# Performance work log

Measured on AMD Instinct MI355X. Metric: run time of the kernel, lower is better.

The kernel has to match this reference:

```python
import jax, jax.numpy as jnp
import numpy as np

N = 100000   # input nodes
M = 100000   # output nodes (size = (N, M))
NNZ = 3_200_000  # edges, avg_degree 32
B = 32       # batch
D = 32       # Kaiming channel dim


def setup_inputs() -> dict:
    key = jax.random.key(0)
    k1, k2, k3 = jax.random.split(key, 3)
    # COO indices: row 0 = src (in [0, N)), row 1 = dst (in [0, M))
    indices = jax.random.randint(k1, (2, NNZ), 0, N, dtype=jnp.int32)
    # Kaiming init: randn * sqrt(2/d), as in the torch module when d is given
    values = jax.random.normal(k2, (NNZ,), dtype=jnp.float32) * np.float32((2.0 / D) ** 0.5)
    bias = jnp.zeros((M, 1), dtype=jnp.float32)
    x = jax.random.normal(k3, (B, N, 1), dtype=jnp.float32)
    return {"x": x, "indices": indices, "values": values, "bias": bias}


def reference(x, indices, values, bias):
    # Equivalent of: for each b, sparse.mm(W.T, x[b]) + bias, W in COO (N, M)
    # y[b, m] = sum_{e: dst[e]==m} values[e] * x[b, src[e]] + bias[m]
    src = indices[0]
    dst = indices[1]
    contrib = x[:, src, 0] * values[None, :]           # (B, NNZ) gather-multiply
    y = jax.ops.segment_sum(contrib.T, dst, num_segments=M)  # (M, B) scatter-add
    return (y.T + bias[:, 0][None, :])[..., None]       # (B, M, 1)
```

## Files before the change

kernel.cpp:

```cpp
#include <hip/hip_runtime.h>
#include <hip/hip_fp16.h>
#include <stdint.h>

#define NB 32
#define BIN_SHIFT 6
#define BIN_ROWS 64
#define NBINS_MAX 2048
#define FCHUNK 8192
#define FTHREADS 1024
#define EPT (FCHUNK / FTHREADS)
#define SRC_BITS 18
#define SRC_MASK ((1u << SRC_BITS) - 1)
#define CAP 2816
#define MAXK 11

__global__ void transpose_x_kernel(const float* __restrict__ x,
                                   __half* __restrict__ xt, int N) {
    __shared__ float tile[32][33];
    int n0 = blockIdx.x * 32;
    for (int i = threadIdx.y; i < 32; i += 8) {
        int n = n0 + threadIdx.x;
        tile[i][threadIdx.x] = (n < N) ? x[(size_t)i * N + n] : 0.f;
    }
    __syncthreads();
    for (int i = threadIdx.y; i < 32; i += 8) {
        int n = n0 + i;
        if (n < N) xt[(size_t)n * NB + threadIdx.x] =
            __float2half(tile[threadIdx.x][i]);
    }
}

__global__ void bin_fill(const int* __restrict__ src,
                         const int* __restrict__ dst,
                         const float* __restrict__ vals,
                         int* __restrict__ binCursor,
                         uint2* __restrict__ csr,
                         int* __restrict__ ovCount,
                         int* __restrict__ ovList,
                         int nnz, int nbins) {
    __shared__ int lhist[NBINS_MAX];
    __shared__ int lbase[NBINS_MAX];
    int t = threadIdx.x;
    int e0 = blockIdx.x * FCHUNK;
    int dcache[EPT];
    for (int i = t; i < nbins; i += FTHREADS) lhist[i] = 0;
    __syncthreads();
#pragma unroll
    for (int k = 0; k < EPT; ++k) {
        int e = e0 + k * FTHREADS + t;
        int d = (e < nnz) ? dst[e] : -1;
        dcache[k] = d;
        if (d >= 0) atomicAdd(&lhist[d >> BIN_SHIFT], 1);
    }
    __syncthreads();
    for (int i = t; i < nbins; i += FTHREADS) {
        int c = lhist[i];
        lbase[i] = c ? atomicAdd(&binCursor[i], c) : 0;
        lhist[i] = 0;
    }
    __syncthreads();
#pragma unroll
    for (int k = 0; k < EPT; ++k) {
        int e = e0 + k * FTHREADS + t;
        int d = dcache[k];
        if (d >= 0) {
            int bin = d >> BIN_SHIFT;
            int r = lbase[bin] + atomicAdd(&lhist[bin], 1);
            if (r < CAP) {
                uint32_t meta = ((uint32_t)(d & (BIN_ROWS - 1)) << SRC_BITS) |
                                (uint32_t)src[e];
                csr[(size_t)bin * CAP + r] =
                    make_uint2(meta, __float_as_uint(vals[e]));
            } else {
                int op = atomicAdd(ovCount, 1);
                ovList[op] = e;
            }
        }
    }
}

__global__ __launch_bounds__(256) void sort_gather(
        const int* __restrict__ binCursor,
        const uint2* __restrict__ csr,
        const __half* __restrict__ xt,
        const float* __restrict__ bias,
        float* __restrict__ out, int M) {
    __shared__ uint2 sorted[CAP];
    __shared__ int rowCnt[BIN_ROWS];
    __shared__ int rowOff[BIN_ROWS];
    int t = threadIdx.x;
    int bin = blockIdx.x;
    int start = bin * CAP;
    int cnt   = min(binCursor[bin], CAP);
    int g = t >> 5;
    int b = t & 31;

    uint2 reg[MAXK];
#pragma unroll
    for (int k = 0; k < MAXK; ++k) {
        int j = t + k * 256;
        if (j < cnt) reg[k] = csr[start + j];
    }
    if (t < BIN_ROWS) rowCnt[t] = 0;
    __syncthreads();
#pragma unroll
    for (int k = 0; k < MAXK; ++k) {
        int j = t + k * 256;
        if (j < cnt) atomicAdd(&rowCnt[reg[k].x >> SRC_BITS], 1);
    }
    __syncthreads();
    if (t == 0) {
        int run = 0;
#pragma unroll
        for (int r = 0; r < BIN_ROWS; ++r) {
            rowOff[r] = run;
            run += rowCnt[r];
        }
    }
    __syncthreads();
#pragma unroll
    for (int k = 0; k < MAXK; ++k) {
        int j = t + k * 256;
        if (j < cnt) {
            int p = atomicAdd(&rowOff[reg[k].x >> SRC_BITS], 1);
            sorted[p] = reg[k];
        }
    }
    __syncthreads();
    for (int r = g; r < BIN_ROWS; r += 8) {
        int m = bin * BIN_ROWS + r;
        if (m >= M) break;
        int jend = rowOff[r];
        int jj   = jend - rowCnt[r];
        float acc0 = 0.f, acc1 = 0.f;
        for (; jj + 8 <= jend; jj += 8) {
            uint2 e0 = sorted[jj + 0];
            uint2 e1 = sorted[jj + 1];
            uint2 e2 = sorted[jj + 2];
            uint2 e3 = sorted[jj + 3];
            uint2 e4 = sorted[jj + 4];
            uint2 e5 = sorted[jj + 5];
            uint2 e6 = sorted[jj + 6];
            uint2 e7 = sorted[jj + 7];
            float x0 = __half2float(xt[(size_t)(e0.x & SRC_MASK) * NB + b]);
            float x1 = __half2float(xt[(size_t)(e1.x & SRC_MASK) * NB + b]);
            float x2 = __half2float(xt[(size_t)(e2.x & SRC_MASK) * NB + b]);
            float x3 = __half2float(xt[(size_t)(e3.x & SRC_MASK) * NB + b]);
            float x4 = __half2float(xt[(size_t)(e4.x & SRC_MASK) * NB + b]);
            float x5 = __half2float(xt[(size_t)(e5.x & SRC_MASK) * NB + b]);
            float x6 = __half2float(xt[(size_t)(e6.x & SRC_MASK) * NB + b]);
            float x7 = __half2float(xt[(size_t)(e7.x & SRC_MASK) * NB + b]);
            acc0 = fmaf(__uint_as_float(e0.y), x0, acc0);
            acc1 = fmaf(__uint_as_float(e1.y), x1, acc1);
            acc0 = fmaf(__uint_as_float(e2.y), x2, acc0);
            acc1 = fmaf(__uint_as_float(e3.y), x3, acc1);
            acc0 = fmaf(__uint_as_float(e4.y), x4, acc0);
            acc1 = fmaf(__uint_as_float(e5.y), x5, acc1);
            acc0 = fmaf(__uint_as_float(e6.y), x6, acc0);
            acc1 = fmaf(__uint_as_float(e7.y), x7, acc1);
        }
        for (; jj < jend; ++jj) {
            uint2 e = sorted[jj];
            acc0 = fmaf(__uint_as_float(e.y),
                        __half2float(xt[(size_t)(e.x & SRC_MASK) * NB + b]),
                        acc0);
        }
        out[(size_t)b * M + m] = acc0 + acc1 + bias[m];
    }
}

__global__ void fixup_kernel(const int* __restrict__ ovCount,
                             const int* __restrict__ ovList,
                             const int* __restrict__ src,
                             const int* __restrict__ dst,
                             const float* __restrict__ vals,
                             const __half* __restrict__ xt,
                             float* __restrict__ out, int M) {
    long long total = (long long)(*ovCount) * 32;
    long long stride = (long long)gridDim.x * blockDim.x;
    for (long long i = (long long)blockIdx.x * blockDim.x + threadIdx.x;
         i < total; i += stride) {
        int k = (int)(i >> 5);
        int b = (int)(i & 31);
        int e = ovList[k];
        atomicAdd(&out[(size_t)b * M + dst[e]],
                  vals[e] * __half2float(xt[(size_t)src[e] * NB + b]));
    }
}

__global__ void finalize_kernel(const float* __restrict__ yt,
                                const float* __restrict__ bias,
                                float* __restrict__ out, int M) {
    __shared__ float tile[32][33];
    int m0 = blockIdx.x * 32;
    for (int i = threadIdx.y; i < 32; i += 8) {
        int m = m0 + i;
        tile[i][threadIdx.x] = (m < M) ? yt[(size_t)m * NB + threadIdx.x] : 0.f;
    }
    __syncthreads();
    for (int i = threadIdx.y; i < 32; i += 8) {
        int m = m0 + threadIdx.x;
        if (m < M) out[(size_t)i * M + m] = tile[threadIdx.x][i] + bias[m];
    }
}

__global__ void scatter_kernel(const int* __restrict__ src,
                               const int* __restrict__ dst,
                               const float* __restrict__ vals,
                               const __half* __restrict__ xt,
                               float* __restrict__ yt, int nnz) {
    long long tid = (long long)blockIdx.x * blockDim.x + threadIdx.x;
    int e = (int)(tid >> 5);
    if (e >= nnz) return;
    int b = (int)(tid & 31);
    atomicAdd(&yt[(size_t)dst[e] * NB + b],
              vals[e] * __half2float(xt[(size_t)src[e] * NB + b]));
}

extern "C" void kernel_launch(void* const* d_in, const int* in_sizes, int n_in,
                              void* d_out, int out_size, void* d_ws, size_t ws_size,
                              hipStream_t stream) {
    const float* x       = (const float*)d_in[0];
    const int*   indices = (const int*)  d_in[1];
    const float* vals    = (const float*)d_in[2];
    const float* bias    = (const float*)d_in[3];

    float* out = (float*)d_out;

    int nnz = in_sizes[1] / 2;
    int N   = in_sizes[0] / NB;
    int M   = in_sizes[3];

    const int* src = indices;
    const int* dst = indices + nnz;

    int nbins = (M + BIN_ROWS - 1) >> BIN_SHIFT;

    __half* xt       = (__half*)d_ws;
    float* yt        = (float*)(xt + (size_t)N * NB);
    int*   binCursor = (int*)(yt + (size_t)M * NB);
    int*   ovCount   = binCursor + NBINS_MAX;
    int*   ovList    = ovCount + 4;
    uint2* csr       = (uint2*)(((uintptr_t)(ovList + nnz) + 15) &
                                ~(uintptr_t)15);

    size_t need = (size_t)((char*)(csr + (size_t)nbins * CAP) - (char*)d_ws);

    transpose_x_kernel<<<(N + 31) / 32, dim3(32, 8), 0, stream>>>(x, xt, N);

    if (ws_size >= need) {
        hipMemsetAsync(binCursor, 0, (NBINS_MAX + 4) * sizeof(int), stream);
        int fgrid = (nnz + FCHUNK - 1) / FCHUNK;
        bin_fill<<<fgrid, FTHREADS, 0, stream>>>(src, dst, vals, binCursor,
                                                 csr, ovCount, ovList,
                                                 nnz, nbins);
        sort_gather<<<nbins, 256, 0, stream>>>(binCursor, csr, xt, bias,
                                               out, M);
        fixup_kernel<<<32, 256, 0, stream>>>(ovCount, ovList, src, dst, vals,
                                             xt, out, M);
    } else {
        hipMemsetAsync(yt, 0, (size_t)M * NB * sizeof(float), stream);
        long long pairs = (long long)nnz * NB;
        int grid = (int)((pairs + 255) / 256);
        scatter_kernel<<<grid, 256, 0, stream>>>(src, dst, vals, xt, yt, nnz);
        finalize_kernel<<<(M + 31) / 32, dim3(32, 8), 0, stream>>>(yt, bias,
                                                                   out, M);
    }
}
```

Measured before the change: 213.9 us.

## Replace global bin cursors with per-block segment offsets and deterministic binning

The fill kernel no longer takes global atomics on per-bin cursors. Each block computes a local exclusive scan of its bin histogram and writes its edges contiguously in its own chunk, plus a per-block offset row. The gather kernel then reads up to 391 small segments per bin and rebuilds the bin's edge list in shared memory. This removes the global atomics, the memset, and the overflow/fixup kernel. The cost is many short, scattered segment reads per bin and a per-thread serial loop over segments, and bins larger than the shared buffer fall back to a shared-memory atomic-accumulate path.

Result: slower. 263.0 us (+22.9%).

```diff
diff --git a/kernel.cpp b/kernel.cpp
--- a/kernel.cpp
+++ b/kernel.cpp
@@ -9,10 +9,10 @@
 #define FCHUNK 8192
 #define FTHREADS 1024
 #define EPT (FCHUNK / FTHREADS)
+#define FGRID_MAX 512
 #define SRC_BITS 18
 #define SRC_MASK ((1u << SRC_BITS) - 1)
 #define CAP 2816
-#define MAXK 11
 
 __global__ void transpose_x_kernel(const float* __restrict__ x,
                                    __half* __restrict__ xt, int N) {
@@ -30,161 +30,181 @@
     }
 }
 
-__global__ void bin_fill(const int* __restrict__ src,
-                         const int* __restrict__ dst,
-                         const float* __restrict__ vals,
-                         int* __restrict__ binCursor,
-                         uint2* __restrict__ csr,
-                         int* __restrict__ ovCount,
-                         int* __restrict__ ovList,
-                         int nnz, int nbins) {
+__global__ void fill_bm(const int* __restrict__ src,
+                        const int* __restrict__ dst,
+                        const float* __restrict__ vals,
+                        uint2* __restrict__ csr,
+                        int* __restrict__ segOff,
+                        int nnz, int nbins) {
     __shared__ int lhist[NBINS_MAX];
     __shared__ int lbase[NBINS_MAX];
+    __shared__ int sscan[FTHREADS];
     int t = threadIdx.x;
-    int e0 = blockIdx.x * FCHUNK;
+    int k = blockIdx.x;
+    int e0 = k * FCHUNK;
+    int chunk = min(FCHUNK, nnz - e0);
     int dcache[EPT];
-    for (int i = t; i < nbins; i += FTHREADS) lhist[i] = 0;
+
+    for (int i = t; i < NBINS_MAX; i += FTHREADS) lhist[i] = 0;
     __syncthreads();
 #pragma unroll
-    for (int k = 0; k < EPT; ++k) {
-        int e = e0 + k * FTHREADS + t;
+    for (int q = 0; q < EPT; ++q) {
+        int e = e0 + q * FTHREADS + t;
         int d = (e < nnz) ? dst[e] : -1;
-        dcache[k] = d;
+        dcache[q] = d;
         if (d >= 0) atomicAdd(&lhist[d >> BIN_SHIFT], 1);
     }
     __syncthreads();
-    for (int i = t; i < nbins; i += FTHREADS) {
-        int c = lhist[i];
-        lbase[i] = c ? atomicAdd(&binCursor[i], c) : 0;
-        lhist[i] = 0;
-    }
-    __syncthreads();
+    int s0 = lhist[2 * t];
+    int s1 = lhist[2 * t + 1];
+    int tsum = s0 + s1;
+    sscan[t] = tsum;
+    __syncthreads();
+    for (int off = 1; off < FTHREADS; off <<= 1) {
+        int add = (t >= off) ? sscan[t - off] : 0;
+        __syncthreads();
+        sscan[t] += add;
+        __syncthreads();
+    }
+    int excl = sscan[t] - tsum;
+    lbase[2 * t]     = excl;
+    lbase[2 * t + 1] = excl + s0;
+    lhist[2 * t]     = 0;
+    lhist[2 * t + 1] = 0;
+    __syncthreads();
+    int* row = segOff + (size_t)k * (nbins + 1);
+    for (int i = t; i <= nbins; i += FTHREADS)
+        row[i] = e0 + ((i < nbins) ? lbase[i] : chunk);
 #pragma unroll
-    for (int k = 0; k < EPT; ++k) {
-        int e = e0 + k * FTHREADS + t;
-        int d = dcache[k];
+    for (int q = 0; q < EPT; ++q) {
+        int e = e0 + q * FTHREADS + t;
+        int d = dcache[q];
         if (d >= 0) {
             int bin = d >> BIN_SHIFT;
             int r = lbase[bin] + atomicAdd(&lhist[bin], 1);
-            if (r < CAP) {
-                uint32_t meta = ((uint32_t)(d & (BIN_ROWS - 1)) << SRC_BITS) |
-                                (uint32_t)src[e];
-                csr[(size_t)bin * CAP + r] =
-                    make_uint2(meta, __float_as_uint(vals[e]));
-            } else {
-                int op = atomicAdd(ovCount, 1);
-                ovList[op] = e;
-            }
+            uint32_t meta = ((uint32_t)(d & (BIN_ROWS - 1)) << SRC_BITS) |
+                            (uint32_t)src[e];
+            csr[e0 + r] = make_uint2(meta, __float_as_uint(vals[e]));
         }
     }
 }
 
 __global__ __launch_bounds__(256) void sort_gather(
-        const int* __restrict__ binCursor,
+        const int* __restrict__ segOff,
         const uint2* __restrict__ csr,
         const __half* __restrict__ xt,
         const float* __restrict__ bias,
-        float* __restrict__ out, int M) {
+        float* __restrict__ out, int M, int nbins, int fgrid) {
     __shared__ uint2 sorted[CAP];
+    __shared__ int segBase[FGRID_MAX];
+    __shared__ short segCnt[FGRID_MAX];
     __shared__ int rowCnt[BIN_ROWS];
     __shared__ int rowOff[BIN_ROWS];
+    __shared__ int totS;
     int t = threadIdx.x;
     int bin = blockIdx.x;
-    int start = bin * CAP;
-    int cnt   = min(binCursor[bin], CAP);
     int g = t >> 5;
     int b = t & 31;
 
-    uint2 reg[MAXK];
+    if (t == 0) totS = 0;
+    if (t < BIN_ROWS) rowCnt[t] = 0;
+    __syncthreads();
+    int mySum = 0;
+    for (int k = t; k < fgrid; k += 256) {
+        const int* row = segOff + (size_t)k * (nbins + 1) + bin;
+        int s0 = row[0];
+        int s1 = row[1];
+        segBase[k] = s0;
+        segCnt[k] = (short)(s1 - s0);
+        mySum += s1 - s0;
+    }
+    if (mySum) atomicAdd(&totS, mySum);
+    __syncthreads();
+    int cnt = totS;
+
+    if (cnt <= CAP) {
+        for (int k = t; k < fgrid; k += 256) {
+            int base = segBase[k], n = segCnt[k];
+            for (int j = 0; j < n; ++j)
+                atomicAdd(&rowCnt[csr[base + j].x >> SRC_BITS], 1);
+        }
+        __syncthreads();
+        if (t == 0) {
+            int run = 0;
 #pragma unroll
-    for (int k = 0; k < MAXK; ++k) {
-        int j = t + k * 256;
-        if (j < cnt) reg[k] = csr[start + j];
-    }
-    if (t < BIN_ROWS) rowCnt[t] = 0;
-    __syncthreads();
-#pragma unroll
-    for (int k = 0; k < MAXK; ++k) {
-        int j = t + k * 256;
-        if (j < cnt) atomicAdd(&rowCnt[reg[k].x >> SRC_BITS], 1);
-    }
-    __syncthreads();
-    if (t == 0) {
-        int run = 0;
-#pragma unroll
-        for (int r = 0; r < BIN_ROWS; ++r) {
-            rowOff[r] = run;
-            run += rowCnt[r];
-        }
-    }
-    __syncthreads();
-#pragma unroll
-    for (int k = 0; k < MAXK; ++k) {
-        int j = t + k * 256;
-        if (j < cnt) {
-            int p = atomicAdd(&rowOff[reg[k].x >> SRC_BITS], 1);
-            sorted[p] = reg[k];
-        }
-    }
-    __syncthreads();
-    for (int r = g; r < BIN_ROWS; r += 8) {
-        int m = bin * BIN_ROWS + r;
-        if (m >= M) break;
-        int jend = rowOff[r];
-        int jj   = jend - rowCnt[r];
-        float acc0 = 0.f, acc1 = 0.f;
-        for (; jj + 8 <= jend; jj += 8) {
-            uint2 e0 = sorted[jj + 0];
-            uint2 e1 = sorted[jj + 1];
-            uint2 e2 = sorted[jj + 2];
-            uint2 e3 = sorted[jj + 3];
-            uint2 e4 = sorted[jj + 4];
-            uint2 e5 = sorted[jj + 5];
-            uint2 e6 = sorted[jj + 6];
-            uint2 e7 = sorted[jj + 7];
-            float x0 = __half2float(xt[(size_t)(e0.x & SRC_MASK) * NB + b]);
-            float x1 = __half2float(xt[(size_t)(e1.x & SRC_MASK) * NB + b]);
-            float x2 = __half2float(xt[(size_t)(e2.x & SRC_MASK) * NB + b]);
-            float x3 = __half2float(xt[(size_t)(e3.x & SRC_MASK) * NB + b]);
-            float x4 = __half2float(xt[(size_t)(e4.x & SRC_MASK) * NB + b]);
-            float x5 = __half2float(xt[(size_t)(e5.x & SRC_MASK) * NB + b]);
-            float x6 = __half2float(xt[(size_t)(e6.x & SRC_MASK) * NB + b]);
-            float x7 = __half2float(xt[(size_t)(e7.x & SRC_MASK) * NB + b]);
-            acc0 = fmaf(__uint_as_float(e0.y), x0, acc0);
-            acc1 = fmaf(__uint_as_float(e1.y), x1, acc1);
-            acc0 = fmaf(__uint_as_float(e2.y), x2, acc0);
-            acc1 = fmaf(__uint_as_float(e3.y), x3, acc1);
-            acc0 = fmaf(__uint_as_float(e4.y), x4, acc0);
-            acc1 = fmaf(__uint_as_float(e5.y), x5, acc1);
-            acc0 = fmaf(__uint_as_float(e6.y), x6, acc0);
-            acc1 = fmaf(__uint_as_float(e7.y), x7, acc1);
-        }
-        for (; jj < jend; ++jj) {
-            uint2 e = sorted[jj];
-            acc0 = fmaf(__uint_as_float(e.y),
-                        __half2float(xt[(size_t)(e.x & SRC_MASK) * NB + b]),
-                        acc0);
-        }
-        out[(size_t)b * M + m] = acc0 + acc1 + bias[m];
-    }
-}
-
-__global__ void fixup_kernel(const int* __restrict__ ovCount,
-                             const int* __restrict__ ovList,
-                             const int* __restrict__ src,
-                             const int* __restrict__ dst,
-                             const float* __restrict__ vals,
-                             const __half* __restrict__ xt,
-                             float* __restrict__ out, int M) {
-    long long total = (long long)(*ovCount) * 32;
-    long long stride = (long long)gridDim.x * blockDim.x;
-    for (long long i = (long long)blockIdx.x * blockDim.x + threadIdx.x;
-         i < total; i += stride) {
-        int k = (int)(i >> 5);
-        int b = (int)(i & 31);
-        int e = ovList[k];
-        atomicAdd(&out[(size_t)b * M + dst[e]],
-                  vals[e] * __half2float(xt[(size_t)src[e] * NB + b]));
+            for (int r = 0; r < BIN_ROWS; ++r) {
+                rowOff[r] = run;
+                run += rowCnt[r];
+            }
+        }
+        __syncthreads();
+        for (int k = t; k < fgrid; k += 256) {
+            int base = segBase[k], n = segCnt[k];
+            for (int j = 0; j < n; ++j) {
+                uint2 e = csr[base + j];
+                int p = atomicAdd(&rowOff[e.x >> SRC_BITS], 1);
+                sorted[p] = e;
+            }
+        }
+        __syncthreads();
+        for (int r = g; r < BIN_ROWS; r += 8) {
+            int m = bin * BIN_ROWS + r;
+            if (m >= M) break;
+            int jend = rowOff[r];
+            int jj   = jend - rowCnt[r];
+            float acc0 = 0.f, acc1 = 0.f;
+            for (; jj + 8 <= jend; jj += 8) {
+                uint2 e0 = sorted[jj + 0];
+                uint2 e1 = sorted[jj + 1];
+                uint2 e2 = sorted[jj + 2];
+                uint2 e3 = sorted[jj + 3];
+                uint2 e4 = sorted[jj + 4];
+                uint2 e5 = sorted[jj + 5];
+                uint2 e6 = sorted[jj + 6];
+                uint2 e7 = sorted[jj + 7];
+                float x0 = __half2float(xt[(size_t)(e0.x & SRC_MASK) * NB + b]);
+                float x1 = __half2float(xt[(size_t)(e1.x & SRC_MASK) * NB + b]);
+                float x2 = __half2float(xt[(size_t)(e2.x & SRC_MASK) * NB + b]);
+                float x3 = __half2float(xt[(size_t)(e3.x & SRC_MASK) * NB + b]);
+                float x4 = __half2float(xt[(size_t)(e4.x & SRC_MASK) * NB + b]);
+                float x5 = __half2float(xt[(size_t)(e5.x & SRC_MASK) * NB + b]);
+                float x6 = __half2float(xt[(size_t)(e6.x & SRC_MASK) * NB + b]);
+                float x7 = __half2float(xt[(size_t)(e7.x & SRC_MASK) * NB + b]);
+                acc0 = fmaf(__uint_as_float(e0.y), x0, acc0);
+                acc1 = fmaf(__uint_as_float(e1.y), x1, acc1);
+                acc0 = fmaf(__uint_as_float(e2.y), x2, acc0);
+                acc1 = fmaf(__uint_as_float(e3.y), x3, acc1);
+                acc0 = fmaf(__uint_as_float(e4.y), x4, acc0);
+                acc1 = fmaf(__uint_as_float(e5.y), x5, acc1);
+                acc0 = fmaf(__uint_as_float(e6.y), x6, acc0);
+                acc1 = fmaf(__uint_as_float(e7.y), x7, acc1);
+            }
+            for (; jj < jend; ++jj) {
+                uint2 e = sorted[jj];
+                acc0 = fmaf(__uint_as_float(e.y),
+                            __half2float(xt[(size_t)(e.x & SRC_MASK) * NB + b]),
+                            acc0);
+            }
+            out[(size_t)b * M + m] = acc0 + acc1 + bias[m];
+        }
+    } else {
+        float* tile = (float*)sorted;
+        for (int i = t; i < BIN_ROWS * NB; i += 256) tile[i] = 0.f;
+        __syncthreads();
+        for (int k = g; k < fgrid; k += 8) {
+            int base = segBase[k], n = segCnt[k];
+            for (int j = 0; j < n; ++j) {
+                uint2 e = csr[base + j];
+                float xv = __half2float(xt[(size_t)(e.x & SRC_MASK) * NB + b]);
+                atomicAdd(&tile[(e.x >> SRC_BITS) * NB + b],
+                          __uint_as_float(e.y) * xv);
+            }
+        }
+        __syncthreads();
+        for (int i = t; i < BIN_ROWS * NB; i += 256) {
+            int m = bin * BIN_ROWS + (i >> 5);
+            if (m < M) out[(size_t)(i & 31) * M + m] = tile[i] + bias[m];
+        }
     }
 }
 
@@ -235,29 +255,23 @@
     const int* dst = indices + nnz;
 
     int nbins = (M + BIN_ROWS - 1) >> BIN_SHIFT;
-
-    __half* xt       = (__half*)d_ws;
-    float* yt        = (float*)(xt + (size_t)N * NB);
-    int*   binCursor = (int*)(yt + (size_t)M * NB);
-    int*   ovCount   = binCursor + NBINS_MAX;
-    int*   ovList    = ovCount + 4;
-    uint2* csr       = (uint2*)(((uintptr_t)(ovList + nnz) + 15) &
-                                ~(uintptr_t)15);
-
-    size_t need = (size_t)((char*)(csr + (size_t)nbins * CAP) - (char*)d_ws);
+    int fgrid = (nnz + FCHUNK - 1) / FCHUNK;
+
+    __half* xt     = (__half*)d_ws;
+    float*  yt     = (float*)(xt + (size_t)N * NB);
+    int*    segOff = (int*)(yt + (size_t)M * NB);
+    uint2*  csr    = (uint2*)(((uintptr_t)(segOff +
+                        (size_t)fgrid * (nbins + 1)) + 15) & ~(uintptr_t)15);
+
+    size_t need = (size_t)((char*)(csr + nnz) - (char*)d_ws);
 
     transpose_x_kernel<<<(N + 31) / 32, dim3(32, 8), 0, stream>>>(x, xt, N);
 
-    if (ws_size >= need) {
-        hipMemsetAsync(binCursor, 0, (NBINS_MAX + 4) * sizeof(int), stream);
-        int fgrid = (nnz + FCHUNK - 1) / FCHUNK;
-        bin_fill<<<fgrid, FTHREADS, 0, stream>>>(src, dst, vals, binCursor,
-                                                 csr, ovCount, ovList,
-                                                 nnz, nbins);
-        sort_gather<<<nbins, 256, 0, stream>>>(binCursor, csr, xt, bias,
-                                               out, M);
-        fixup_kernel<<<32, 256, 0, stream>>>(ovCount, ovList, src, dst, vals,
-                                             xt, out, M);
+    if (ws_size >= need && fgrid <= FGRID_MAX && nbins <= NBINS_MAX) {
+        fill_bm<<<fgrid, FTHREADS, 0, stream>>>(src, dst, vals, csr, segOff,
+                                                nnz, nbins);
+        sort_gather<<<nbins, 256, 0, stream>>>(segOff, csr, xt, bias, out,
+                                               M, nbins, fgrid);
     } else {
         hipMemsetAsync(yt, 0, (size_t)M * NB * sizeof(float), stream);
         long long pairs = (long long)nnz * NB;
```

## Replace single-pass fine binning with two-level coarse/fine radix partition

Applied to the files above, without the earlier changes.

Edges are first scattered into 1024-row coarse buckets while per-64-row fine counts are accumulated. A scan turns those counts into exact offsets, and a second pass scatters each coarse bucket into a compact fine CSR. This is meant to reduce global atomic contention and scattered-write inefficiency from binning straight into 1563 fixed-capacity bins. It adds two kernel launches and an extra read/write pass over all edges. sort_gather gains an atomic shared-tile fallback for bins above capacity, replacing the overflow path for fine bins.

New measurement: 198.1 us. 1.08x faster.

```diff
diff --git a/kernel.cpp b/kernel.cpp
--- a/kernel.cpp
+++ b/kernel.cpp
@@ -6,13 +6,21 @@
 #define BIN_SHIFT 6
 #define BIN_ROWS 64
 #define NBINS_MAX 2048
+#define CSHIFT 10
+#define NC_MAX 128
+#define FPC 16
 #define FCHUNK 8192
 #define FTHREADS 1024
 #define EPT (FCHUNK / FTHREADS)
+#define CAP_C 34816
+#define P2CHUNK 8192
+#define CH2 ((CAP_C + P2CHUNK - 1) / P2CHUNK)
+#define EPT2 (P2CHUNK / FTHREADS)
 #define SRC_BITS 18
 #define SRC_MASK ((1u << SRC_BITS) - 1)
 #define CAP 2816
 #define MAXK 11
+
 
 __global__ void transpose_x_kernel(const float* __restrict__ x,
                                    __half* __restrict__ xt, int N) {
@@ -30,57 +38,133 @@
     }
 }
 
-__global__ void bin_fill(const int* __restrict__ src,
-                         const int* __restrict__ dst,
-                         const float* __restrict__ vals,
-                         int* __restrict__ binCursor,
-                         uint2* __restrict__ csr,
-                         int* __restrict__ ovCount,
-                         int* __restrict__ ovList,
-                         int nnz, int nbins) {
-    __shared__ int lhist[NBINS_MAX];
-    __shared__ int lbase[NBINS_MAX];
+__global__ void fill_coarse(const int* __restrict__ src,
+                            const int* __restrict__ dst,
+                            const float* __restrict__ vals,
+                            int* __restrict__ cCursor,
+                            uint2* __restrict__ cCsr,
+                            int* __restrict__ fineCnt,
+                            int* __restrict__ ovCount,
+                            int* __restrict__ ovList,
+                            int nnz, int ncoarse, int nbins) {
+    __shared__ int lhist[NC_MAX];
+    __shared__ int lbase[NC_MAX];
+    __shared__ int fh[NBINS_MAX];
     int t = threadIdx.x;
     int e0 = blockIdx.x * FCHUNK;
     int dcache[EPT];
-    for (int i = t; i < nbins; i += FTHREADS) lhist[i] = 0;
-    __syncthreads();
-#pragma unroll
-    for (int k = 0; k < EPT; ++k) {
-        int e = e0 + k * FTHREADS + t;
+    for (int i = t; i < NC_MAX; i += FTHREADS) lhist[i] = 0;
+    for (int i = t; i < nbins; i += FTHREADS) fh[i] = 0;
+    __syncthreads();
+#pragma unroll
+    for (int q = 0; q < EPT; ++q) {
+        int e = e0 + q * FTHREADS + t;
         int d = (e < nnz) ? dst[e] : -1;
-        dcache[k] = d;
-        if (d >= 0) atomicAdd(&lhist[d >> BIN_SHIFT], 1);
-    }
-    __syncthreads();
-    for (int i = t; i < nbins; i += FTHREADS) {
+        dcache[q] = d;
+        if (d >= 0) atomicAdd(&lhist[d >> CSHIFT], 1);
+    }
+    __syncthreads();
+    for (int i = t; i < ncoarse; i += FTHREADS) {
         int c = lhist[i];
-        lbase[i] = c ? atomicAdd(&binCursor[i], c) : 0;
+        lbase[i] = c ? atomicAdd(&cCursor[i], c) : 0;
         lhist[i] = 0;
     }
     __syncthreads();
 #pragma unroll
-    for (int k = 0; k < EPT; ++k) {
-        int e = e0 + k * FTHREADS + t;
-        int d = dcache[k];
+    for (int q = 0; q < EPT; ++q) {
+        int e = e0 + q * FTHREADS + t;
+        int d = dcache[q];
         if (d >= 0) {
-            int bin = d >> BIN_SHIFT;
-            int r = lbase[bin] + atomicAdd(&lhist[bin], 1);
-            if (r < CAP) {
-                uint32_t meta = ((uint32_t)(d & (BIN_ROWS - 1)) << SRC_BITS) |
+            int c = d >> CSHIFT;
+            int r = lbase[c] + atomicAdd(&lhist[c], 1);
+            if (r < CAP_C) {
+                uint32_t meta = ((uint32_t)(d & 1023) << SRC_BITS) |
                                 (uint32_t)src[e];
-                csr[(size_t)bin * CAP + r] =
+                cCsr[(size_t)c * CAP_C + r] =
                     make_uint2(meta, __float_as_uint(vals[e]));
+                atomicAdd(&fh[d >> BIN_SHIFT], 1);
             } else {
                 int op = atomicAdd(ovCount, 1);
                 ovList[op] = e;
             }
         }
     }
+    __syncthreads();
+    for (int i = t; i < nbins; i += FTHREADS)
+        if (fh[i]) atomicAdd(&fineCnt[i], fh[i]);
+}
+
+__global__ void fine_scan(const int* __restrict__ fineCnt,
+                          int* __restrict__ fineBase,
+                          int* __restrict__ fineCursor, int nbins) {
+    __shared__ int s[1024];
+    int t = threadIdx.x;
+    int i0 = t * 2, i1 = t * 2 + 1;
+    int v0 = (i0 < nbins) ? fineCnt[i0] : 0;
+    int v1 = (i1 < nbins) ? fineCnt[i1] : 0;
+    int sum = v0 + v1;
+    s[t] = sum;
+    __syncthreads();
+    for (int off = 1; off < 1024; off <<= 1) {
+        int add = (t >= off) ? s[t - off] : 0;
+        __syncthreads();
+        s[t] += add;
+        __syncthreads();
+    }
+    int run = s[t] - sum;
+    if (i0 < nbins) { fineBase[i0] = run; fineCursor[i0] = run; }
+    run += v0;
+    if (i1 < nbins) { fineBase[i1] = run; fineCursor[i1] = run; }
+}
+
+__global__ void fill_fine(const int* __restrict__ cCursor,
+                          const uint2* __restrict__ cCsr,
+                          int* __restrict__ fineCursor,
+                          uint2* __restrict__ fineCsr) {
+    __shared__ int lhist[FPC];
+    __shared__ int lbase[FPC];
+    int c = blockIdx.x / CH2;
+    int i = blockIdx.x % CH2;
+    int n  = min(cCursor[c], CAP_C);
+    int j0 = i * P2CHUNK;
+    int jn = min(j0 + P2CHUNK, n);
+    if (j0 >= jn) return;
+    int t = threadIdx.x;
+    uint2 ecache[EPT2];
+    if (t < FPC) lhist[t] = 0;
+    __syncthreads();
+    const uint2* reg = cCsr + (size_t)c * CAP_C;
+#pragma unroll
+    for (int q = 0; q < EPT2; ++q) {
+        int j = j0 + q * FTHREADS + t;
+        if (j < jn) {
+            uint2 e = reg[j];
+            ecache[q] = e;
+            atomicAdd(&lhist[(e.x >> 24) & 15], 1);
+        }
+    }
+    __syncthreads();
+    if (t < FPC) {
+        int cn = lhist[t];
+        lbase[t] = cn ? atomicAdd(&fineCursor[c * FPC + t], cn) : 0;
+        lhist[t] = 0;
+    }
+    __syncthreads();
+#pragma unroll
+    for (int q = 0; q < EPT2; ++q) {
+        int j = j0 + q * FTHREADS + t;
+        if (j < jn) {
+            uint2 e = ecache[q];
+            int f = (e.x >> 24) & 15;
+            int p = lbase[f] + atomicAdd(&lhist[f], 1);
+            fineCsr[p] = e;
+        }
+    }
 }
 
 __global__ __launch_bounds__(256) void sort_gather(
-        const int* __restrict__ binCursor,
+        const int* __restrict__ fineBase,
+        const int* __restrict__ fineCursor,
         const uint2* __restrict__ csr,
         const __half* __restrict__ xt,
         const float* __restrict__ bias,
@@ -90,82 +174,100 @@
     __shared__ int rowOff[BIN_ROWS];
     int t = threadIdx.x;
     int bin = blockIdx.x;
-    int start = bin * CAP;
-    int cnt   = min(binCursor[bin], CAP);
+    int start = fineBase[bin];
+    int cnt   = fineCursor[bin] - start;
     int g = t >> 5;
     int b = t & 31;
 
-    uint2 reg[MAXK];
-#pragma unroll
-    for (int k = 0; k < MAXK; ++k) {
-        int j = t + k * 256;
-        if (j < cnt) reg[k] = csr[start + j];
-    }
-    if (t < BIN_ROWS) rowCnt[t] = 0;
-    __syncthreads();
-#pragma unroll
-    for (int k = 0; k < MAXK; ++k) {
-        int j = t + k * 256;
-        if (j < cnt) atomicAdd(&rowCnt[reg[k].x >> SRC_BITS], 1);
-    }
-    __syncthreads();
-    if (t == 0) {
-        int run = 0;
-#pragma unroll
-        for (int r = 0; r < BIN_ROWS; ++r) {
-            rowOff[r] = run;
-            run += rowCnt[r];
-        }
-    }
-    __syncthreads();
-#pragma unroll
-    for (int k = 0; k < MAXK; ++k) {
-        int j = t + k * 256;
-        if (j < cnt) {
-            int p = atomicAdd(&rowOff[reg[k].x >> SRC_BITS], 1);
-            sorted[p] = reg[k];
-        }
-    }
-    __syncthreads();
-    for (int r = g; r < BIN_ROWS; r += 8) {
-        int m = bin * BIN_ROWS + r;
-        if (m >= M) break;
-        int jend = rowOff[r];
-        int jj   = jend - rowCnt[r];
-        float acc0 = 0.f, acc1 = 0.f;
-        for (; jj + 8 <= jend; jj += 8) {
-            uint2 e0 = sorted[jj + 0];
-            uint2 e1 = sorted[jj + 1];
-            uint2 e2 = sorted[jj + 2];
-            uint2 e3 = sorted[jj + 3];
-            uint2 e4 = sorted[jj + 4];
-            uint2 e5 = sorted[jj + 5];
-            uint2 e6 = sorted[jj + 6];
-            uint2 e7 = sorted[jj + 7];
-            float x0 = __half2float(xt[(size_t)(e0.x & SRC_MASK) * NB + b]);
-            float x1 = __half2float(xt[(size_t)(e1.x & SRC_MASK) * NB + b]);
-            float x2 = __half2float(xt[(size_t)(e2.x & SRC_MASK) * NB + b]);
-            float x3 = __half2float(xt[(size_t)(e3.x & SRC_MASK) * NB + b]);
-            float x4 = __half2float(xt[(size_t)(e4.x & SRC_MASK) * NB + b]);
-            float x5 = __half2float(xt[(size_t)(e5.x & SRC_MASK) * NB + b]);
-            float x6 = __half2float(xt[(size_t)(e6.x & SRC_MASK) * NB + b]);
-            float x7 = __half2float(xt[(size_t)(e7.x & SRC_MASK) * NB + b]);
-            acc0 = fmaf(__uint_as_float(e0.y), x0, acc0);
-            acc1 = fmaf(__uint_as_float(e1.y), x1, acc1);
-            acc0 = fmaf(__uint_as_float(e2.y), x2, acc0);
-            acc1 = fmaf(__uint_as_float(e3.y), x3, acc1);
-            acc0 = fmaf(__uint_as_float(e4.y), x4, acc0);
-            acc1 = fmaf(__uint_as_float(e5.y), x5, acc1);
-            acc0 = fmaf(__uint_as_float(e6.y), x6, acc0);
-            acc1 = fmaf(__uint_as_float(e7.y), x7, acc1);
-        }
-        for (; jj < jend; ++jj) {
-            uint2 e = sorted[jj];
-            acc0 = fmaf(__uint_as_float(e.y),
-                        __half2float(xt[(size_t)(e.x & SRC_MASK) * NB + b]),
-                        acc0);
-        }
-        out[(size_t)b * M + m] = acc0 + acc1 + bias[m];
+    if (cnt <= CAP) {
+        uint2 reg[MAXK];
+#pragma unroll
+        for (int k = 0; k < MAXK; ++k) {
+            int j = t + k * 256;
+            if (j < cnt) reg[k] = csr[start + j];
+        }
+        if (t < BIN_ROWS) rowCnt[t] = 0;
+        __syncthreads();
+#pragma unroll
+        for (int k = 0; k < MAXK; ++k) {
+            int j = t + k * 256;
+            if (j < cnt)
+                atomicAdd(&rowCnt[(reg[k].x >> SRC_BITS) & 63], 1);
+        }
+        __syncthreads();
+        if (t == 0) {
+            int run = 0;
+#pragma unroll
+            for (int r = 0; r < BIN_ROWS; ++r) {
+                rowOff[r] = run;
+                run += rowCnt[r];
+            }
+        }
+        __syncthreads();
+#pragma unroll
+        for (int k = 0; k < MAXK; ++k) {
+            int j = t + k * 256;
+            if (j < cnt) {
+                int p = atomicAdd(&rowOff[(reg[k].x >> SRC_BITS) & 63], 1);
+                sorted[p] = reg[k];
+            }
+        }
+        __syncthreads();
+        for (int r = g; r < BIN_ROWS; r += 8) {
+            int m = bin * BIN_ROWS + r;
+            if (m >= M) break;
+            int jend = rowOff[r];
+            int jj   = jend - rowCnt[r];
+            float acc0 = 0.f, acc1 = 0.f;
+            for (; jj + 8 <= jend; jj += 8) {
+                uint2 e0 = sorted[jj + 0];
+                uint2 e1 = sorted[jj + 1];
+                uint2 e2 = sorted[jj + 2];
+                uint2 e3 = sorted[jj + 3];
+                uint2 e4 = sorted[jj + 4];
+                uint2 e5 = sorted[jj + 5];
+                uint2 e6 = sorted[jj + 6];
+                uint2 e7 = sorted[jj + 7];
+                float x0 = __half2float(xt[(size_t)(e0.x & SRC_MASK) * NB + b]);
+                float x1 = __half2float(xt[(size_t)(e1.x & SRC_MASK) * NB + b]);
+                float x2 = __half2float(xt[(size_t)(e2.x & SRC_MASK) * NB + b]);
+                float x3 = __half2float(xt[(size_t)(e3.x & SRC_MASK) * NB + b]);
+                float x4 = __half2float(xt[(size_t)(e4.x & SRC_MASK) * NB + b]);
+                float x5 = __half2float(xt[(size_t)(e5.x & SRC_MASK) * NB + b]);
+                float x6 = __half2float(xt[(size_t)(e6.x & SRC_MASK) * NB + b]);
+                float x7 = __half2float(xt[(size_t)(e7.x & SRC_MASK) * NB + b]);
+                acc0 = fmaf(__uint_as_float(e0.y), x0, acc0);
+                acc1 = fmaf(__uint_as_float(e1.y), x1, acc1);
+                acc0 = fmaf(__uint_as_float(e2.y), x2, acc0);
+                acc1 = fmaf(__uint_as_float(e3.y), x3, acc1);
+                acc0 = fmaf(__uint_as_float(e4.y), x4, acc0);
+                acc1 = fmaf(__uint_as_float(e5.y), x5, acc1);
+                acc0 = fmaf(__uint_as_float(e6.y), x6, acc0);
+                acc1 = fmaf(__uint_as_float(e7.y), x7, acc1);
+            }
+            for (; jj < jend; ++jj) {
+                uint2 e = sorted[jj];
+                acc0 = fmaf(__uint_as_float(e.y),
+                            __half2float(xt[(size_t)(e.x & SRC_MASK) * NB + b]),
+                            acc0);
+            }
+            out[(size_t)b * M + m] = acc0 + acc1 + bias[m];
+        }
+    } else {
+        float* tile = (float*)sorted;
+        for (int i = t; i < BIN_ROWS * NB; i += 256) tile[i] = 0.f;
+        __syncthreads();
+        for (int j = start + g; j < start + cnt; j += 8) {
+            uint2 e = csr[j];
+            float xv = __half2float(xt[(size_t)(e.x & SRC_MASK) * NB + b]);
+            atomicAdd(&tile[((e.x >> SRC_BITS) & 63) * NB + b],
+                      __uint_as_float(e.y) * xv);
+        }
+        __syncthreads();
+        for (int i = t; i < BIN_ROWS * NB; i += 256) {
+            int m = bin * BIN_ROWS + (i >> 5);
+            if (m < M) out[(size_t)(i & 31) * M + m] = tile[i] + bias[m];
+        }
     }
 }
 
@@ -234,31 +336,44 @@
     const int* src = indices;
     const int* dst = indices + nnz;
 
-    int nbins = (M + BIN_ROWS - 1) >> BIN_SHIFT;
-
-    __half* xt       = (__half*)d_ws;
-    float* yt        = (float*)(xt + (size_t)N * NB);
-    int*   binCursor = (int*)(yt + (size_t)M * NB);
-    int*   ovCount   = binCursor + NBINS_MAX;
-    int*   ovList    = ovCount + 4;
-    uint2* csr       = (uint2*)(((uintptr_t)(ovList + nnz) + 15) &
-                                ~(uintptr_t)15);
-
-    size_t need = (size_t)((char*)(csr + (size_t)nbins * CAP) - (char*)d_ws);
+    int nbins   = (M + BIN_ROWS - 1) >> BIN_SHIFT;
+    int ncoarse = (M + (1 << CSHIFT) - 1) >> CSHIFT;
+
+    __half* xt         = (__half*)d_ws;
+    int*    fineCnt    = (int*)(xt + (size_t)N * NB);
+    int*    cCursor    = fineCnt + NBINS_MAX;
+    int*    ovCount    = cCursor + NC_MAX;
+    int*    fineBase   = ovCount + 4;
+    int*    fineCursor = fineBase + NBINS_MAX;
+    int*    ovList     = fineCursor + NBINS_MAX;
+    uint2*  cCsr       = (uint2*)(((uintptr_t)(ovList + nnz) + 15) &
+                                  ~(uintptr_t)15);
+    uint2*  fineCsr    = cCsr + (size_t)ncoarse * CAP_C;
+
+    size_t need = (size_t)((char*)(fineCsr + nnz) - (char*)d_ws);
+
+    float* yt = (float*)(xt + (size_t)N * NB);
+    size_t need_fb = (size_t)((char*)(yt + (size_t)M * NB) - (char*)d_ws);
 
     transpose_x_kernel<<<(N + 31) / 32, dim3(32, 8), 0, stream>>>(x, xt, N);
 
-    if (ws_size >= need) {
-        hipMemsetAsync(binCursor, 0, (NBINS_MAX + 4) * sizeof(int), stream);
+    if (ws_size >= need && nbins <= NBINS_MAX && ncoarse <= NC_MAX) {
+        hipMemsetAsync(fineCnt, 0, (NBINS_MAX + NC_MAX + 4) * sizeof(int),
+                       stream);
         int fgrid = (nnz + FCHUNK - 1) / FCHUNK;
-        bin_fill<<<fgrid, FTHREADS, 0, stream>>>(src, dst, vals, binCursor,
-                                                 csr, ovCount, ovList,
-                                                 nnz, nbins);
-        sort_gather<<<nbins, 256, 0, stream>>>(binCursor, csr, xt, bias,
-                                               out, M);
+        fill_coarse<<<fgrid, FTHREADS, 0, stream>>>(src, dst, vals, cCursor,
+                                                    cCsr, fineCnt, ovCount,
+                                                    ovList, nnz, ncoarse,
+                                                    nbins);
+        fine_scan<<<1, 1024, 0, stream>>>(fineCnt, fineBase, fineCursor,
+                                          nbins);
+        fill_fine<<<ncoarse * CH2, FTHREADS, 0, stream>>>(cCursor, cCsr,
+                                                          fineCursor, fineCsr);
+        sort_gather<<<nbins, 256, 0, stream>>>(fineBase, fineCursor, fineCsr,
+                                               xt, bias, out, M);
         fixup_kernel<<<32, 256, 0, stream>>>(ovCount, ovList, src, dst, vals,
                                              xt, out, M);
-    } else {
+    } else if (ws_size >= need_fb) {
         hipMemsetAsync(yt, 0, (size_t)M * NB * sizeof(float), stream);
         long long pairs = (long long)nnz * NB;
         int grid = (int)((pairs + 255) / 256);
```
